# Kernel optimization log

Hardware: AMD Instinct MI355X
Metric: run time of the kernel (lower is better)

## Reference

```python
import jax, jax.numpy as jnp
import numpy as np

EPSILON = 1e-15
CUTOFF = 5.0
N_RBF = 16           # num_radial_filters -> RBF dim = 2*16+1 = 33
SCALE = 8            # _quadrature_points_per_atom_scaling


def poly_envelope_5_2(x):
    # e3nn.poly_envelope(5, 2): f'(x) ~ x^5 (1-x)^2, f(0)=1, f(1)=0
    x2 = x * x
    x6 = x2 * x2 * x2
    f = 1.0 - 28.0 * x6 + 48.0 * x6 * x - 21.0 * x6 * x2
    return jnp.where(x < 1.0, f, jnp.zeros_like(x))


def sin_cos_basis(r, n_rbf):
    r = r[..., None]                                  # [A,T,1]
    k = jnp.arange(1, n_rbf + 1, dtype=r.dtype)       # [n_rbf]
    return jnp.sqrt(2.0) * jnp.concatenate(
        [0.1 * jnp.ones_like(r), jnp.sin(k * jnp.pi * r), jnp.cos(k * jnp.pi * r)],
        axis=-1,
    )                                                 # [A,T,2*n_rbf+1]


def spherical_harmonics_l012_norm(d):
    # Real spherical harmonics up to l=2, e3nn m-ordering, normalization='norm'
    # (each l-block has unit norm for unit input directions).
    x, y, z = d[..., 0], d[..., 1], d[..., 2]
    r2 = x * x + y * y + z * z
    s3 = jnp.sqrt(3.0)
    one = jnp.ones_like(x)
    return jnp.stack(
        [
            one,                       # l=0
            y, z, x,                   # l=1 (m=-1,0,1)
            s3 * x * y,                # l=2 m=-2
            s3 * y * z,                # l=2 m=-1
            0.5 * (3.0 * z * z - r2),  # l=2 m=0
            s3 * x * z,                # l=2 m=1
            0.5 * s3 * (x * x - y * y) # l=2 m=2
        ],
        axis=-1,
    )                                  # [A,T,9]


def setup_inputs() -> dict:
    key = jax.random.key(0)
    k1, k2, k3, k4 = jax.random.split(key, 4)
    A, N = 64, 200000
    nuc_pos = 4.0 * jax.random.normal(k1, (A, 3), dtype=jnp.float32)
    grid_coords = 4.0 * jax.random.normal(k2, (N, 3), dtype=jnp.float32)
    weights = jax.random.uniform(k3, (N,), dtype=jnp.float32)
    n = jax.random.uniform(k4, (N,), dtype=jnp.float32)
    atom_mask = jnp.ones((A,), dtype=bool)
    return {"nuc_pos": nuc_pos, "atom_mask": atom_mask,
            "grid_coords": grid_coords, "weights": weights, "n": n}


def reference(nuc_pos, atom_mask, grid_coords, weights, n):
    g = grid_coords / CUTOFF                          # [N,3]
    p = nuc_pos / CUTOFF                              # [A,3]
    diff = p[:, None] - g[None]                       # [A,N,3]
    dist = jnp.linalg.norm(diff, axis=-1)             # [A,N]
    A, N = dist.shape
    T = min(N, SCALE * N // A)                        # static
    idx = jnp.argsort(dist, axis=1)[:, :T]            # [A,T] nearest grid points
    diff = jnp.take_along_axis(diff, idx[:, :, None], axis=1)   # [A,T,3]
    dist = jnp.take_along_axis(dist, idx, axis=1)                # [A,T]
    n_t = n[idx]                                      # [A,T]
    w_t = weights[idx]                                # [A,T]
    rbf = sin_cos_basis(dist, N_RBF) * poly_envelope_5_2(dist)[..., None]  # [A,T,33]
    dirs = diff / (dist[..., None] + EPSILON)         # [A,T,3]
    sh = spherical_harmonics_l012_norm(dirs)          # [A,T,9]
    node_feats = jnp.einsum('atr,ath,at,at->arh', rbf, sh, n_t, w_t)  # [A,33,9]
    return node_feats
```

## Files before the change

kernel.cpp:

```cpp
#include <hip/hip_runtime.h>


typedef float f32x4 __attribute__((ext_vector_type(4)));
typedef int   i32x4 __attribute__((ext_vector_type(4)));

#define SLICES 32
#define NB1    256
#define NB2    512
#define CLAMP0 4000u
#define CHA    2
#define NCHUNK (SLICES * CHA)
#define PBSTR  304
#define CUT25  0x41C80000u

__device__ __forceinline__ unsigned d2bits(float px, float py, float pz,
                                           float gx, float gy, float gz) {
  float dx = px - gx, dy = py - gy, dz = pz - gz;
  float d2 = __fmaf_rn(dx, dx, __fmaf_rn(dy, dy, __fmul_rn(dz, dz)));
  return __float_as_uint(d2);
}

__device__ __forceinline__ unsigned short tobf(float v) {
  return (unsigned short)((__float_as_uint(v) + 0x8000u) >> 16);
}

__device__ __forceinline__ void mfma_acc(f32x4& d, i32x4 a, i32x4 b) {
  asm("v_mfma_f32_16x16x32_bf16 %0, %1, %2, %0" : "+v"(d) : "v"(a), "v"(b));
}

__global__ __launch_bounds__(256, 8) void enc_hist_store(
    const float* __restrict__ nuc, const float* __restrict__ grid, int N,
    unsigned* __restrict__ hists, unsigned* __restrict__ cnt,
    uint2* __restrict__ pairs, int scap, unsigned* __restrict__ ghist2) {
  __shared__ unsigned lh[NB1];
  __shared__ unsigned s_cnt;
  int a = blockIdx.x / SLICES, s = blockIdx.x % SLICES;
  int tid = threadIdx.x, lane = tid & 63;
  if (tid < NB1) lh[tid] = 0;
  if (tid == 0) s_cnt = 0;
  {
    const int stripe = NB2 / SLICES;
    if (tid < stripe) ghist2[(size_t)a * NB2 + s * stripe + tid] = 0;
  }
  __syncthreads();

  float px = nuc[3*a+0], py = nuc[3*a+1], pz = nuc[3*a+2];
  uint2* seg = pairs + (size_t)blockIdx.x * scap;
  const float4* G4 = (const float4*)grid;
  int nq = N >> 2;
  int qper = (nq + SLICES - 1) / SLICES;
  int qlo = s * qper, qhi = min(nq, qlo + qper);

  for (int qi = qlo + tid; qi < qhi; qi += 256) {
    float4 A4 = G4[3*qi], B4 = G4[3*qi+1], C4 = G4[3*qi+2];
    float xs[4] = {A4.x, A4.w, B4.z, C4.y};
    float ys[4] = {A4.y, B4.x, B4.w, C4.z};
    float zs[4] = {A4.z, B4.y, C4.x, C4.w};
    unsigned bt[4];
    #pragma unroll
    for (int k = 0; k < 4; ++k) {
      bt[k] = d2bits(px, py, pz, xs[k], ys[k], zs[k]);
      if (bt[k] < CUT25) {
        int cb = (int)(bt[k] >> 18) - (int)CLAMP0;
        atomicAdd(&lh[cb > 0 ? cb : 0], 1u);
      }
    }
    #pragma unroll
    for (int k = 0; k < 4; ++k) {
      bool sel = bt[k] < CUT25;
      unsigned long long mm = __ballot(sel);
      if (mm) {
        int leader = __ffsll(mm) - 1;
        unsigned base = 0;
        if (lane == leader) base = atomicAdd(&s_cnt, (unsigned)__popcll(mm));
        base = __shfl(base, leader);
        if (sel) {
          unsigned pos = base + (unsigned)__popcll(mm & ((1ull << lane) - 1ull));
          if (pos < (unsigned)scap) seg[pos] = make_uint2(bt[k], (unsigned)(4*qi + k));
        }
      }
    }
  }
  if (s == SLICES - 1) {
    for (int i = 4*nq + tid; i < N; i += 256) {
      unsigned bits = d2bits(px, py, pz, grid[3*i+0], grid[3*i+1], grid[3*i+2]);
      bool sel = bits < CUT25;
      if (sel) {
        int cb = (int)(bits >> 18) - (int)CLAMP0;
        atomicAdd(&lh[cb > 0 ? cb : 0], 1u);
      }
      unsigned long long mm = __ballot(sel);
      if (mm) {
        int leader = __ffsll(mm) - 1;
        unsigned base = 0;
        if (lane == leader) base = atomicAdd(&s_cnt, (unsigned)__popcll(mm));
        base = __shfl(base, leader);
        if (sel) {
          unsigned pos = base + (unsigned)__popcll(mm & ((1ull << lane) - 1ull));
          if (pos < (unsigned)scap) seg[pos] = make_uint2(bits, (unsigned)i);
        }
      }
    }
  }
  __syncthreads();
  if (tid < NB1) hists[(size_t)blockIdx.x * NB1 + tid] = lh[tid];
  if (tid == 0) cnt[blockIdx.x] = s_cnt;
}

__global__ __launch_bounds__(256, 8) void enc_fine(
    const unsigned* __restrict__ hists, const unsigned* __restrict__ cnt,
    const uint2* __restrict__ pairs, int scap, unsigned T,
    unsigned* __restrict__ b1r, unsigned* __restrict__ r2r,
    unsigned* __restrict__ ghist2) {
  __shared__ unsigned lh[NB1];
  __shared__ unsigned s_bin, s_pre;
  int seg_id = blockIdx.x;
  int a = seg_id / SLICES, s = seg_id % SLICES;
  int tid = threadIdx.x;
  if (tid < NB1) {
    unsigned acc = 0;
    const unsigned* base = hists + (size_t)a * SLICES * NB1 + tid;
    #pragma unroll 8
    for (int t = 0; t < SLICES; ++t) acc += base[(size_t)t * NB1];
    lh[tid] = acc;
  }
  if (tid == 0) { s_bin = NB1 - 1; s_pre = 0; }
  __syncthreads();
  if (tid < 64) {
    int lane = tid, base = 4 * lane;
    unsigned h0 = lh[base], h1 = lh[base+1], h2 = lh[base+2], h3 = lh[base+3];
    unsigned ssum = h0 + h1 + h2 + h3;
    unsigned p = ssum;
    #pragma unroll
    for (int d = 1; d < 64; d <<= 1) {
      unsigned t = __shfl_up(p, d);
      if (lane >= d) p += t;
    }
    unsigned excl = p - ssum;
    if (excl < T && T <= p) {
      unsigned cum = excl;
      unsigned hh[4] = {h0, h1, h2, h3};
      #pragma unroll
      for (int k = 0; k < 4; ++k) {
        if (cum + hh[k] >= T) { s_bin = (unsigned)(base + k); s_pre = cum; break; }
        cum += hh[k];
      }
    }
  }
  __syncthreads();
  unsigned b1c = s_bin;
  if (s == 0 && tid == 0) { b1r[a] = s_bin; r2r[a] = T - s_pre; }

  unsigned tb1 = b1c + CLAMP0;
  int total = min((int)cnt[seg_id], scap);
  const uint2* seg = pairs + (size_t)seg_id * scap;
  unsigned* gh2 = ghist2 + (size_t)a * NB2;
  for (int i = tid; i < total; i += 256) {
    uint2 p = seg[i];
    unsigned cb = p.x >> 18;
    bool match = b1c ? (cb == tb1) : (cb <= CLAMP0);
    if (match) atomicAdd(&gh2[(p.x >> 9) & (NB2 - 1)], 1u);
  }
}

__global__ __launch_bounds__(256, 4) void enc_accum(
    const float* __restrict__ nuc, const float* __restrict__ grid,
    const float* __restrict__ wv, const float* __restrict__ nv,
    const unsigned* __restrict__ b1r, const unsigned* __restrict__ r2r,
    const unsigned* __restrict__ ghist2, const unsigned* __restrict__ cnt,
    const uint2* __restrict__ pairs, int scap, float* __restrict__ pb) {
  __shared__ __align__(16) unsigned short lds[4][4608];
  __shared__ unsigned lh2[NB2];
  __shared__ unsigned s_bin2;
  int seg_id = blockIdx.x / CHA, c = blockIdx.x % CHA;
  int a = seg_id / SLICES;
  int tid = threadIdx.x, lane = tid & 63, w = tid >> 6;
  unsigned short* SB = &lds[w][0];

  {
    i32x4 z = {0, 0, 0, 0};
    i32x4* zp = (i32x4*)SB;
    #pragma unroll
    for (int t = 0; t < 9; ++t) zp[lane + t * 64] = z;
  }
  {
    const unsigned* gh2 = ghist2 + (size_t)a * NB2;
    lh2[tid] = gh2[tid];
    lh2[tid + 256] = gh2[tid + 256];
  }
  if (tid == 0) s_bin2 = NB2 - 1;
  __syncthreads();
  unsigned R = r2r[a];
  if (tid < 64) {
    int lane2 = tid, base = 8 * lane2;
    unsigned hh[8], ssum = 0;
    #pragma unroll
    for (int k = 0; k < 8; ++k) { hh[k] = lh2[base + k]; ssum += hh[k]; }
    unsigned p = ssum;
    #pragma unroll
    for (int d = 1; d < 64; d <<= 1) {
      unsigned t = __shfl_up(p, d);
      if (lane2 >= d) p += t;
    }
    unsigned excl = p - ssum;
    if (excl < R && R <= p) {
      unsigned cum = excl;
      #pragma unroll
      for (int k = 0; k < 8; ++k) {
        if (cum + hh[k] >= R) { s_bin2 = (unsigned)(base + k); break; }
        cum += hh[k];
      }
    }
  }
  __syncthreads();
  unsigned thr = ((b1r[a] + CLAMP0) << 9) | s_bin2;

  float px = nuc[3*a+0], py = nuc[3*a+1], pz = nuc[3*a+2];
  int total = min((int)cnt[seg_id], scap);
  const uint2* lst = pairs + (size_t)seg_id * scap;

  f32x4 acc0 = {0,0,0,0}, acc1 = {0,0,0,0}, acc2 = {0,0,0,0};
  int m = lane & 15, q = lane >> 4;
  const float SQRT2 = 1.41421356237309515f;
  const float PIF   = 3.14159265358979323846f;
  const float S3    = 1.73205080756887729f;

  for (int jb = c * 256 + w * 64; jb < total; jb += CHA * 256) {
    int j = jb + lane;
    bool valid = j < total;
    uint2 pr = valid ? lst[j] : make_uint2(0xFFFFFFFFu, 0u);
    bool live = valid && ((pr.x >> 9) <= thr);
    unsigned gi = pr.y;
    if (live) {
      float gx = grid[3*gi+0], gy = grid[3*gi+1], gz = grid[3*gi+2];
      float dx = px - gx, dy = py - gy, dz = pz - gz;
      float d2 = __fmaf_rn(dx, dx, __fmaf_rn(dy, dy, dz * dz));
#if __has_builtin(__builtin_amdgcn_sqrtf)
      float rn = __builtin_amdgcn_sqrtf(d2) * 0.2f;
#else
      float rn = sqrtf(d2) * 0.2f;
#endif
      float x2 = rn * rn;
      float x6 = x2 * x2 * x2;
      float e  = __fmaf_rn(x6, __fmaf_rn(-21.f, x2, __fmaf_rn(48.f, rn, -28.f)), 1.f);
      float f  = SQRT2 * e;
      float nw = nv[gi] * wv[gi];
#if __has_builtin(__builtin_amdgcn_rcpf)
      float inv = 0.2f * __builtin_amdgcn_rcpf(rn + 1e-15f);
#else
      float inv = 0.2f / (rn + 1e-15f);
#endif
      float X = dx * inv, Y = dy * inv, Z = dz * inv;
      float r2 = __fmaf_rn(X, X, __fmaf_rn(Y, Y, Z * Z));
      SB[3456 + 0*72 + lane] = tobf(nw);
      SB[3456 + 1*72 + lane] = tobf(nw * Y);
      SB[3456 + 2*72 + lane] = tobf(nw * Z);
      SB[3456 + 3*72 + lane] = tobf(nw * X);
      SB[3456 + 4*72 + lane] = tobf(nw * S3 * X * Y);
      SB[3456 + 5*72 + lane] = tobf(nw * S3 * Y * Z);
      SB[3456 + 6*72 + lane] = tobf(nw * 0.5f * __fmaf_rn(3.f, Z * Z, -r2));
      SB[3456 + 7*72 + lane] = tobf(nw * S3 * X * Z);
      SB[3456 + 8*72 + lane] = tobf(nw * 0.5f * S3 * (X * X - Y * Y));
      float s1 = __sinf(PIF * rn), c1 = __cosf(PIF * rn);
      SB[0 * 72 + lane]  = tobf(0.1f * f);
      float sk = s1, ck = c1;
      SB[1 * 72 + lane]  = tobf(f * sk);
      SB[17 * 72 + lane] = tobf(f * ck);
      #pragma unroll
      for (int k = 2; k <= 16; ++k) {
        float sn = __fmaf_rn(sk, c1, ck * s1);
        float cn = __fmaf_rn(ck, c1, -(sk * s1));
        sk = sn; ck = cn;
        SB[k * 72 + lane]        = tobf(f * sk);
        SB[(16 + k) * 72 + lane] = tobf(f * ck);
      }
    } else {
      #pragma unroll
      for (int h = 0; h < 9; ++h) SB[3456 + h * 72 + lane] = 0;
    }
    #pragma unroll
    for (int g = 0; g < 2; ++g) {
      int cb = 8 * q + 32 * g;
      i32x4 bf = *(const i32x4*)&SB[3456 + m * 72 + cb];
      i32x4 a0 = *(const i32x4*)&SB[(0  + m) * 72 + cb];
      mfma_acc(acc0, a0, bf);
      i32x4 a1 = *(const i32x4*)&SB[(16 + m) * 72 + cb];
      mfma_acc(acc1, a1, bf);
      i32x4 a2 = *(const i32x4*)&SB[(32 + m) * 72 + cb];
      mfma_acc(acc2, a2, bf);
    }
  }
  asm volatile("s_nop 7\n\ts_nop 7" : "+v"(acc0), "+v"(acc1), "+v"(acc2));

  float* redw = (float*)&lds[w][0];
  if (m < 9) {
    #pragma unroll
    for (int t = 0; t < 4; ++t) {
      int row = 4 * q + t;
      redw[(row +  0) * 9 + m] = acc0[t];
      redw[(row + 16) * 9 + m] = acc1[t];
      if (row + 32 < 33) redw[(row + 32) * 9 + m] = acc2[t];
    }
  }
  __syncthreads();
  float* pbb = pb + (size_t)blockIdx.x * PBSTR;
  for (int v = tid; v < 297; v += 256) {
    float s0 = ((const float*)&lds[0][0])[v] + ((const float*)&lds[1][0])[v];
    float s1 = ((const float*)&lds[2][0])[v] + ((const float*)&lds[3][0])[v];
    pbb[v] = s0 + s1;
  }
}

__global__ __launch_bounds__(256) void enc_reduce(
    const float* __restrict__ pb, float* __restrict__ out, int nout) {
  int idx = blockIdx.x * 256 + threadIdx.x;
  if (idx >= nout) return;
  int a = idx / 297, v = idx - a * 297;
  const float* p = pb + (size_t)a * NCHUNK * PBSTR + v;
  float s = 0.f;
  #pragma unroll 8
  for (int k = 0; k < NCHUNK; ++k) s += p[(size_t)k * PBSTR];
  out[idx] = s;
}

extern "C" void kernel_launch(void* const* d_in, const int* in_sizes, int n_in,
                              void* d_out, int out_size, void* d_ws, size_t ws_size,
                              hipStream_t stream) {
  const float* nuc  = (const float*)d_in[0];
  const float* grid = (const float*)d_in[2];
  const float* wts  = (const float*)d_in[3];
  const float* nn   = (const float*)d_in[4];
  int A = in_sizes[0] / 3;
  int N = in_sizes[2] / 3;
  long long t8 = (8LL * (long long)N) / (long long)A;
  unsigned T = (unsigned)(t8 < (long long)N ? t8 : (long long)N);

  unsigned* ws     = (unsigned*)d_ws;
  unsigned* cnt    = ws;
  unsigned* b1r    = cnt + A * SLICES;
  unsigned* r2r    = b1r + A;
  unsigned* hists  = r2r + A;
  unsigned* ghist2 = hists + (size_t)A * SLICES * NB1;
  float*    pb     = (float*)(ghist2 + (size_t)A * NB2);
  uint2*    pairs  = (uint2*)(pb + (size_t)A * SLICES * CHA * PBSTR);

  int nq   = N >> 2;
  int qper = (nq + SLICES - 1) / SLICES;
  int SCAP = qper * 4 + 4;
  {
    long long head  = (long long)(((unsigned*)pairs) - ws);
    long long avail = (long long)(ws_size / 4) - head;
    long long need  = 2LL * SCAP * A * SLICES;
    if (avail > 0 && need > avail) SCAP = (int)(avail / (2LL * A * SLICES));
  }
  float* out = (float*)d_out;
  int nout = A * 297;

  enc_hist_store<<<A * SLICES,         256, 0, stream>>>(nuc, grid, N, hists, cnt,
                                                         pairs, SCAP, ghist2);
  enc_fine      <<<A * SLICES,         256, 0, stream>>>(hists, cnt, pairs, SCAP, T,
                                                         b1r, r2r, ghist2);
  enc_accum     <<<A * SLICES * CHA,   256, 0, stream>>>(nuc, grid, wts, nn, b1r, r2r,
                                                         ghist2, cnt, pairs, SCAP, pb);
  enc_reduce    <<<(nout + 255) / 256, 256, 0, stream>>>(pb, out, nout);
}
```

Baseline: 64.86 us.

## Store precomputed displacement and weight records instead of indices to avoid gathers

The first pass now writes a 16-byte record per candidate: squared distance, the displacement packed as fp16, and the product n*w, replacing the old (distance, index) pair. The accumulate kernel reads these records directly instead of gathering grid coordinates, weights and densities by index, so it no longer does random global loads. In exchange the scatter buffer doubles in size, the first pass has to read every weight and density value, and the fine-histogram pass uses a strided read. The fp16 displacement lowers the precision of the direction vectors, and sin and cos now come from a single sincos call. Launch-bound occupancy hints were also removed from two kernels.

Result: no change. 64.83 us (-0.1%).

```diff
diff --git a/kernel.cpp b/kernel.cpp
--- a/kernel.cpp
+++ b/kernel.cpp
@@ -1,4 +1,5 @@
 #include <hip/hip_runtime.h>
+#include <hip/hip_fp16.h>
 
 
 typedef float f32x4 __attribute__((ext_vector_type(4)));
@@ -13,25 +14,24 @@
 #define PBSTR  304
 #define CUT25  0x41C80000u
 
-__device__ __forceinline__ unsigned d2bits(float px, float py, float pz,
-                                           float gx, float gy, float gz) {
-  float dx = px - gx, dy = py - gy, dz = pz - gz;
-  float d2 = __fmaf_rn(dx, dx, __fmaf_rn(dy, dy, __fmul_rn(dz, dz)));
-  return __float_as_uint(d2);
-}
-
 __device__ __forceinline__ unsigned short tobf(float v) {
   return (unsigned short)((__float_as_uint(v) + 0x8000u) >> 16);
 }
 
+__device__ __forceinline__ unsigned pack2h(float a, float b) {
+  __half2 h = __floats2half2_rn(a, b);
+  return *reinterpret_cast<unsigned*>(&h);
+}
+
 __device__ __forceinline__ void mfma_acc(f32x4& d, i32x4 a, i32x4 b) {
   asm("v_mfma_f32_16x16x32_bf16 %0, %1, %2, %0" : "+v"(d) : "v"(a), "v"(b));
 }
 
-__global__ __launch_bounds__(256, 8) void enc_hist_store(
-    const float* __restrict__ nuc, const float* __restrict__ grid, int N,
+__global__ __launch_bounds__(256) void enc_hist_store(
+    const float* __restrict__ nuc, const float* __restrict__ grid,
+    const float* __restrict__ wv, const float* __restrict__ nv, int N,
     unsigned* __restrict__ hists, unsigned* __restrict__ cnt,
-    uint2* __restrict__ pairs, int scap, unsigned* __restrict__ ghist2) {
+    uint4* __restrict__ recs, int scap, unsigned* __restrict__ ghist2) {
   __shared__ unsigned lh[NB1];
   __shared__ unsigned s_cnt;
   int a = blockIdx.x / SLICES, s = blockIdx.x % SLICES;
@@ -45,21 +45,29 @@
   __syncthreads();
 
   float px = nuc[3*a+0], py = nuc[3*a+1], pz = nuc[3*a+2];
-  uint2* seg = pairs + (size_t)blockIdx.x * scap;
+  uint4* seg = recs + (size_t)blockIdx.x * scap;
   const float4* G4 = (const float4*)grid;
+  const float4* W4 = (const float4*)wv;
+  const float4* V4 = (const float4*)nv;
   int nq = N >> 2;
   int qper = (nq + SLICES - 1) / SLICES;
   int qlo = s * qper, qhi = min(nq, qlo + qper);
 
   for (int qi = qlo + tid; qi < qhi; qi += 256) {
     float4 A4 = G4[3*qi], B4 = G4[3*qi+1], C4 = G4[3*qi+2];
+    float4 w4 = W4[qi], v4 = V4[qi];
     float xs[4] = {A4.x, A4.w, B4.z, C4.y};
     float ys[4] = {A4.y, B4.x, B4.w, C4.z};
     float zs[4] = {A4.z, B4.y, C4.x, C4.w};
+    float nws[4] = {v4.x * w4.x, v4.y * w4.y, v4.z * w4.z, v4.w * w4.w};
+    float dxs[4], dys[4], dzs[4];
     unsigned bt[4];
     #pragma unroll
     for (int k = 0; k < 4; ++k) {
-      bt[k] = d2bits(px, py, pz, xs[k], ys[k], zs[k]);
+      float dx = px - xs[k], dy = py - ys[k], dz = pz - zs[k];
+      dxs[k] = dx; dys[k] = dy; dzs[k] = dz;
+      float d2 = __fmaf_rn(dx, dx, __fmaf_rn(dy, dy, __fmul_rn(dz, dz)));
+      bt[k] = __float_as_uint(d2);
       if (bt[k] < CUT25) {
         int cb = (int)(bt[k] >> 18) - (int)CLAMP0;
         atomicAdd(&lh[cb > 0 ? cb : 0], 1u);
@@ -76,14 +84,23 @@
         base = __shfl(base, leader);
         if (sel) {
           unsigned pos = base + (unsigned)__popcll(mm & ((1ull << lane) - 1ull));
-          if (pos < (unsigned)scap) seg[pos] = make_uint2(bt[k], (unsigned)(4*qi + k));
+          if (pos < (unsigned)scap) {
+            uint4 r;
+            r.x = bt[k];
+            r.y = pack2h(dxs[k], dys[k]);
+            r.z = pack2h(dzs[k], 0.f);
+            r.w = __float_as_uint(nws[k]);
+            seg[pos] = r;
+          }
         }
       }
     }
   }
   if (s == SLICES - 1) {
     for (int i = 4*nq + tid; i < N; i += 256) {
-      unsigned bits = d2bits(px, py, pz, grid[3*i+0], grid[3*i+1], grid[3*i+2]);
+      float dx = px - grid[3*i+0], dy = py - grid[3*i+1], dz = pz - grid[3*i+2];
+      float d2 = __fmaf_rn(dx, dx, __fmaf_rn(dy, dy, __fmul_rn(dz, dz)));
+      unsigned bits = __float_as_uint(d2);
       bool sel = bits < CUT25;
       if (sel) {
         int cb = (int)(bits >> 18) - (int)CLAMP0;
@@ -97,7 +114,14 @@
         base = __shfl(base, leader);
         if (sel) {
           unsigned pos = base + (unsigned)__popcll(mm & ((1ull << lane) - 1ull));
-          if (pos < (unsigned)scap) seg[pos] = make_uint2(bits, (unsigned)i);
+          if (pos < (unsigned)scap) {
+            uint4 r;
+            r.x = bits;
+            r.y = pack2h(dx, dy);
+            r.z = pack2h(dz, 0.f);
+            r.w = __float_as_uint(nv[i] * wv[i]);
+            seg[pos] = r;
+          }
         }
       }
     }
@@ -107,9 +131,9 @@
   if (tid == 0) cnt[blockIdx.x] = s_cnt;
 }
 
-__global__ __launch_bounds__(256, 8) void enc_fine(
+__global__ __launch_bounds__(256) void enc_fine(
     const unsigned* __restrict__ hists, const unsigned* __restrict__ cnt,
-    const uint2* __restrict__ pairs, int scap, unsigned T,
+    const uint4* __restrict__ recs, int scap, unsigned T,
     unsigned* __restrict__ b1r, unsigned* __restrict__ r2r,
     unsigned* __restrict__ ghist2) {
   __shared__ unsigned lh[NB1];
@@ -153,22 +177,20 @@
 
   unsigned tb1 = b1c + CLAMP0;
   int total = min((int)cnt[seg_id], scap);
-  const uint2* seg = pairs + (size_t)seg_id * scap;
+  const unsigned* segb = (const unsigned*)(recs + (size_t)seg_id * scap);
   unsigned* gh2 = ghist2 + (size_t)a * NB2;
   for (int i = tid; i < total; i += 256) {
-    uint2 p = seg[i];
-    unsigned cb = p.x >> 18;
+    unsigned bits = segb[4 * i];
+    unsigned cb = bits >> 18;
     bool match = b1c ? (cb == tb1) : (cb <= CLAMP0);
-    if (match) atomicAdd(&gh2[(p.x >> 9) & (NB2 - 1)], 1u);
+    if (match) atomicAdd(&gh2[(bits >> 9) & (NB2 - 1)], 1u);
   }
 }
 
 __global__ __launch_bounds__(256, 4) void enc_accum(
-    const float* __restrict__ nuc, const float* __restrict__ grid,
-    const float* __restrict__ wv, const float* __restrict__ nv,
     const unsigned* __restrict__ b1r, const unsigned* __restrict__ r2r,
     const unsigned* __restrict__ ghist2, const unsigned* __restrict__ cnt,
-    const uint2* __restrict__ pairs, int scap, float* __restrict__ pb) {
+    const uint4* __restrict__ recs, int scap, float* __restrict__ pb) {
   __shared__ __align__(16) unsigned short lds[4][4608];
   __shared__ unsigned lh2[NB2];
   __shared__ unsigned s_bin2;
@@ -215,9 +237,8 @@
   __syncthreads();
   unsigned thr = ((b1r[a] + CLAMP0) << 9) | s_bin2;
 
-  float px = nuc[3*a+0], py = nuc[3*a+1], pz = nuc[3*a+2];
   int total = min((int)cnt[seg_id], scap);
-  const uint2* lst = pairs + (size_t)seg_id * scap;
+  const uint4* lst = recs + (size_t)seg_id * scap;
 
   f32x4 acc0 = {0,0,0,0}, acc1 = {0,0,0,0}, acc2 = {0,0,0,0};
   int m = lane & 15, q = lane >> 4;
@@ -228,13 +249,15 @@
   for (int jb = c * 256 + w * 64; jb < total; jb += CHA * 256) {
     int j = jb + lane;
     bool valid = j < total;
-    uint2 pr = valid ? lst[j] : make_uint2(0xFFFFFFFFu, 0u);
+    uint4 pr;
+    if (valid) pr = lst[j]; else pr.x = 0xFFFFFFFFu;
     bool live = valid && ((pr.x >> 9) <= thr);
-    unsigned gi = pr.y;
     if (live) {
-      float gx = grid[3*gi+0], gy = grid[3*gi+1], gz = grid[3*gi+2];
-      float dx = px - gx, dy = py - gy, dz = pz - gz;
-      float d2 = __fmaf_rn(dx, dx, __fmaf_rn(dy, dy, dz * dz));
+      float d2 = __uint_as_float(pr.x);
+      __half2 hxy = *reinterpret_cast<const __half2*>(&pr.y);
+      __half2 hz2 = *reinterpret_cast<const __half2*>(&pr.z);
+      float dx = __low2float(hxy), dy = __high2float(hxy), dz = __low2float(hz2);
+      float nw = __uint_as_float(pr.w);
 #if __has_builtin(__builtin_amdgcn_sqrtf)
       float rn = __builtin_amdgcn_sqrtf(d2) * 0.2f;
 #else
@@ -244,7 +267,6 @@
       float x6 = x2 * x2 * x2;
       float e  = __fmaf_rn(x6, __fmaf_rn(-21.f, x2, __fmaf_rn(48.f, rn, -28.f)), 1.f);
       float f  = SQRT2 * e;
-      float nw = nv[gi] * wv[gi];
 #if __has_builtin(__builtin_amdgcn_rcpf)
       float inv = 0.2f * __builtin_amdgcn_rcpf(rn + 1e-15f);
 #else
@@ -261,7 +283,8 @@
       SB[3456 + 6*72 + lane] = tobf(nw * 0.5f * __fmaf_rn(3.f, Z * Z, -r2));
       SB[3456 + 7*72 + lane] = tobf(nw * S3 * X * Z);
       SB[3456 + 8*72 + lane] = tobf(nw * 0.5f * S3 * (X * X - Y * Y));
-      float s1 = __sinf(PIF * rn), c1 = __cosf(PIF * rn);
+      float s1, c1;
+      __sincosf(PIF * rn, &s1, &c1);
       SB[0 * 72 + lane]  = tobf(0.1f * f);
       float sk = s1, ck = c1;
       SB[1 * 72 + lane]  = tobf(f * sk);
@@ -342,25 +365,25 @@
   unsigned* hists  = r2r + A;
   unsigned* ghist2 = hists + (size_t)A * SLICES * NB1;
   float*    pb     = (float*)(ghist2 + (size_t)A * NB2);
-  uint2*    pairs  = (uint2*)(pb + (size_t)A * SLICES * CHA * PBSTR);
+  uint4*    recs   = (uint4*)(pb + (size_t)A * SLICES * CHA * PBSTR);
 
   int nq   = N >> 2;
   int qper = (nq + SLICES - 1) / SLICES;
   int SCAP = qper * 4 + 4;
   {
-    long long head  = (long long)(((unsigned*)pairs) - ws);
+    long long head  = (long long)(((unsigned*)recs) - ws);
     long long avail = (long long)(ws_size / 4) - head;
-    long long need  = 2LL * SCAP * A * SLICES;
-    if (avail > 0 && need > avail) SCAP = (int)(avail / (2LL * A * SLICES));
+    long long need  = 4LL * SCAP * A * SLICES;
+    if (avail > 0 && need > avail) SCAP = (int)(avail / (4LL * A * SLICES));
   }
   float* out = (float*)d_out;
   int nout = A * 297;
 
-  enc_hist_store<<<A * SLICES,         256, 0, stream>>>(nuc, grid, N, hists, cnt,
-                                                         pairs, SCAP, ghist2);
-  enc_fine      <<<A * SLICES,         256, 0, stream>>>(hists, cnt, pairs, SCAP, T,
+  enc_hist_store<<<A * SLICES,         256, 0, stream>>>(nuc, grid, wts, nn, N, hists,
+                                                         cnt, recs, SCAP, ghist2);
+  enc_fine      <<<A * SLICES,         256, 0, stream>>>(hists, cnt, recs, SCAP, T,
                                                          b1r, r2r, ghist2);
-  enc_accum     <<<A * SLICES * CHA,   256, 0, stream>>>(nuc, grid, wts, nn, b1r, r2r,
-                                                         ghist2, cnt, pairs, SCAP, pb);
+  enc_accum     <<<A * SLICES * CHA,   256, 0, stream>>>(b1r, r2r, ghist2, cnt,
+                                                         recs, SCAP, pb);
   enc_reduce    <<<(nout + 255) / 256, 256, 0, stream>>>(pb, out, nout);
 }
```
